# Kernel tuning notes

Hardware: AMD Instinct MI355X
Metric: run time of the kernel (lower is better)

The kernel has to match this reference:

```python
import jax, jax.numpy as jnp
import numpy as np

N_NODES = 100_000
N_EDGES = 1_200_000
IN_C, HID_C, OUT_C, K = 64, 64, 32, 3


def setup_inputs() -> dict:
    key = jax.random.key(0)
    ks = jax.random.split(key, 8)
    x = jax.random.normal(ks[0], (N_NODES, IN_C), dtype=jnp.float32)
    edge_index = jax.random.randint(ks[1], (2, N_EDGES), 0, N_NODES, dtype=jnp.int64)
    # ChebConv parameters: weight [K, in, out], bias [out] (Glorot-ish scale)
    W1 = jax.random.normal(ks[2], (K, IN_C, HID_C), dtype=jnp.float32) / np.sqrt(IN_C)
    b1 = jnp.zeros((HID_C,), dtype=jnp.float32)
    W2 = jax.random.normal(ks[3], (K, HID_C, OUT_C), dtype=jnp.float32) / np.sqrt(HID_C)
    b2 = jnp.zeros((OUT_C,), dtype=jnp.float32)
    return {"x": x, "edge_index": edge_index, "W1": W1, "b1": b1, "W2": W2, "b2": b2}


def _cheb_conv(x, row, col, norm_w, W, b):
    # Scaled Laplacian with lambda_max=2 (PyG default): L_hat = -D^{-1/2} A D^{-1/2}
    def prop(t):  # L_hat @ t, via edge gather + segment-sum scatter
        msg = norm_w[:, None] * t[col]            # [E, C]
        return -jax.ops.segment_sum(msg, row, num_segments=N_NODES)

    Tx0 = x
    out = Tx0 @ W[0]
    Tx1 = prop(x)
    out = out + Tx1 @ W[1]
    for k in range(2, W.shape[0]):
        Tx2 = 2.0 * prop(Tx1) - Tx0          # Chebyshev recurrence
        out = out + Tx2 @ W[k]
        Tx0, Tx1 = Tx1, Tx2
    return out + b


def reference(x, edge_index, W1, b1, W2, b2):
    row, col = edge_index[0], edge_index[1]
    deg = jax.ops.segment_sum(jnp.ones((row.shape[0],), x.dtype), row,
                              num_segments=N_NODES)
    deg_inv_sqrt = jnp.where(deg > 0, jax.lax.rsqrt(jnp.maximum(deg, 1.0)), 0.0)
    norm_w = deg_inv_sqrt[row] * deg_inv_sqrt[col]   # symmetric normalization

    h = jax.nn.relu(_cheb_conv(x, row, col, norm_w, W1, b1))
    # dropout omitted (eval mode / training=False)
    return _cheb_conv(h, row, col, norm_w, W2, b2)
```

## Files before the change

kernel.cpp:

```cpp
#include <hip/hip_runtime.h>
#include <hip/hip_fp16.h>

#define N_NODES_C 100000
#define N_EDGES_C 1200000
#define NBUK ((N_NODES_C + 255) >> 8)
#define CHUNK 4096

typedef _Float16 f16x8 __attribute__((ext_vector_type(8)));
typedef float f32x4 __attribute__((ext_vector_type(4)));

#define PACK(r8, c) ((c) | ((r8) << 17))
#define UNPACK_C(v) ((v) & 0x1FFFF)
#define UNPACK_R(v) ((v) >> 17)

__global__ __launch_bounds__(256) void hist_f2h(const int* __restrict__ ei,
                                                int* __restrict__ bucket_cnt,
                                                const float* __restrict__ x,
                                                __half* __restrict__ xh,
                                                int nedges, int n4, int histB) {
    __shared__ int cnt[NBUK];
    const int tid = threadIdx.x;
    if (blockIdx.x < histB) {
        const int base = blockIdx.x * CHUNK;
        const int nloc = min(CHUNK, nedges - base);
        for (int i = tid; i < NBUK; i += 256) cnt[i] = 0;
        __syncthreads();
        for (int i = tid; i < nloc; i += 256) atomicAdd(&cnt[ei[base + i] >> 8], 1);
        __syncthreads();
        for (int b = tid; b < NBUK; b += 256) {
            int n = cnt[b];
            if (n) atomicAdd(&bucket_cnt[b], n);
        }
    } else {
        int i = (blockIdx.x - histB) * 256 + tid;
        if (i < n4) {
            float4 v = ((const float4*)x)[i];
            __half2 tmp[2];
            tmp[0] = __floats2half2_rn(v.x, v.y);
            tmp[1] = __floats2half2_rn(v.z, v.w);
            ((float2*)xh)[i] = *(float2*)tmp;
        }
    }
}

__global__ __launch_bounds__(256) void scan_fold(const int* __restrict__ bucket_cnt,
                                                 int* __restrict__ bucket_base,
                                                 int* __restrict__ bucket_next, int nb,
                                                 const float* __restrict__ W1,
                                                 const float* __restrict__ W2,
                                                 __half* __restrict__ W1f,
                                                 __half* __restrict__ W2f) {
    const int tid = threadIdx.x;
    if (blockIdx.x == 0) {
        __shared__ int s[256];
        int a0 = (2 * tid < nb) ? bucket_cnt[2 * tid] : 0;
        int a1 = (2 * tid + 1 < nb) ? bucket_cnt[2 * tid + 1] : 0;
        s[tid] = a0 + a1;
        __syncthreads();
        for (int off = 1; off < 256; off <<= 1) {
            int v = s[tid];
            int add = (tid >= off) ? s[tid - off] : 0;
            __syncthreads();
            s[tid] = v + add;
            __syncthreads();
        }
        int excl = (tid > 0) ? s[tid - 1] : 0;
        if (2 * tid < nb) { bucket_base[2 * tid] = excl; bucket_next[2 * tid] = excl; }
        if (2 * tid + 1 < nb) { bucket_base[2 * tid + 1] = excl + a0; bucket_next[2 * tid + 1] = excl + a0; }
        if (tid == 255) bucket_base[nb] = s[255];
        return;
    }
    int i = (blockIdx.x - 1) * 256 + tid;
    if (i < 12288) {
        int j = i & 7;
        int lane = (i >> 3) & 63;
        int rest = i >> 9;
        int kh = rest % 6;
        int ct = rest / 6;
        int term = kh >> 1;
        int k = ((kh & 1) << 5) | ((lane >> 4) << 3) | j;
        int c = (ct << 4) | (lane & 15);
        float w0 = W1[k * 64 + c];
        float w1 = W1[4096 + k * 64 + c];
        float w2 = W1[2 * 4096 + k * 64 + c];
        float v = (term == 0) ? (w0 - w2) : ((term == 1) ? w1 : 2.0f * w2);
        W1f[i] = __float2half(v);
    } else if (i < 12288 + 6144) {
        int ii = i - 12288;
        int j = ii & 7;
        int lane = (ii >> 3) & 63;
        int rest = ii >> 9;
        int kh = rest & 1;
        int ct = rest >> 1;
        int k = (kh << 5) | ((lane >> 4) << 3) | j;
        int cg = ct * 16 + (lane & 15);
        int seg = cg >> 5;
        int c = cg & 31;
        float w0 = W2[k * 32 + c];
        float w1 = W2[2048 + k * 32 + c];
        float w2 = W2[2 * 2048 + k * 32 + c];
        float v = (seg == 0) ? (w0 - w2) : ((seg == 1) ? w1 : 2.0f * w2);
        W2f[ii] = __float2half(v);
    }
}

__global__ __launch_bounds__(256) void bin_stage(const int* __restrict__ ei,
                                                 int* __restrict__ bucket_next,
                                                 int* __restrict__ staged, int nedges) {
    __shared__ int cnt[NBUK];
    __shared__ int ofs[NBUK];
    __shared__ int run[NBUK];
    __shared__ int gbase[NBUK];
    __shared__ int ssum[256];
    __shared__ int2 sedge[CHUNK];
    const int tid = threadIdx.x;
    const int base = blockIdx.x * CHUNK;
    const int nloc = min(CHUNK, nedges - base);

    for (int i = tid; i < NBUK; i += 256) { cnt[i] = 0; run[i] = 0; }
    __syncthreads();

    int r[16], c[16];
#pragma unroll
    for (int k = 0; k < 16; ++k) {
        int loc = tid + k * 256;
        bool ok = loc < nloc;
        int idx = base + loc;
        r[k] = ok ? ei[idx] : -1;
        c[k] = ok ? ei[nedges + idx] : 0;
        if (ok) atomicAdd(&cnt[r[k] >> 8], 1);
    }
    __syncthreads();

    int a0 = (2 * tid < NBUK) ? cnt[2 * tid] : 0;
    int a1 = (2 * tid + 1 < NBUK) ? cnt[2 * tid + 1] : 0;
    ssum[tid] = a0 + a1;
    __syncthreads();
    for (int off = 1; off < 256; off <<= 1) {
        int v = ssum[tid];
        int add = (tid >= off) ? ssum[tid - off] : 0;
        __syncthreads();
        ssum[tid] = v + add;
        __syncthreads();
    }
    int excl = (tid > 0) ? ssum[tid - 1] : 0;
    if (2 * tid < NBUK) ofs[2 * tid] = excl;
    if (2 * tid + 1 < NBUK) ofs[2 * tid + 1] = excl + a0;
    __syncthreads();

#pragma unroll
    for (int k = 0; k < 16; ++k) {
        if (r[k] >= 0) {
            int b = r[k] >> 8;
            int p = atomicAdd(&run[b], 1);
            sedge[ofs[b] + p] = make_int2(r[k], c[k]);
        }
    }
    __syncthreads();

    for (int b = tid; b < NBUK; b += 256) {
        int n = cnt[b];
        gbase[b] = n ? atomicAdd(&bucket_next[b], n) : 0;
    }
    __syncthreads();

    for (int i = tid; i < nloc; i += 256) {
        int2 e = sedge[i];
        int b = e.x >> 8;
        staged[gbase[b] + (i - ofs[b])] = PACK(e.x & 255, e.y);
    }
}

__global__ __launch_bounds__(256) void bin_count(const int* __restrict__ staged,
                                                 const int* __restrict__ bucket_base,
                                                 int* __restrict__ rowptr, float* __restrict__ dis,
                                                 int nnodes, int nedges) {
    __shared__ int deg[256];
    __shared__ int ssum[256];
    const int b = blockIdx.x;
    const int n0 = b << 8;
    const int nend = min(n0 + 256, nnodes);
    const int nloc = nend - n0;
    const int tid = threadIdx.x;
    deg[tid] = 0;
    __syncthreads();
    const int ebase = bucket_base[b];
    const int ecount = bucket_base[b + 1] - ebase;
    for (int i = tid; i < ecount; i += 256) {
        atomicAdd(&deg[UNPACK_R(staged[ebase + i])], 1);
    }
    __syncthreads();
    int d = deg[tid];
    if (tid < nloc) {
        float df = (float)d;
        dis[n0 + tid] = (d > 0) ? (1.0f / sqrtf(fmaxf(df, 1.f))) : 0.f;
    }
    ssum[tid] = d;
    __syncthreads();
    for (int off = 1; off < 256; off <<= 1) {
        int v = ssum[tid];
        int add = (tid >= off) ? ssum[tid - off] : 0;
        __syncthreads();
        ssum[tid] = v + add;
        __syncthreads();
    }
    int excl = (tid > 0) ? ssum[tid - 1] : 0;
    if (tid < nloc) rowptr[n0 + tid] = ebase + excl;
    if (b == NBUK - 1 && tid == 0) rowptr[nnodes] = nedges;
}

__global__ __launch_bounds__(256) void bin_place(const int* __restrict__ staged,
                                                 const int* __restrict__ rowptr,
                                                 const float* __restrict__ dis,
                                                 int2* __restrict__ colw, int nnodes) {
    __shared__ int rp[256];
    __shared__ int nx[256];
    __shared__ float dl[256];
    const int b = blockIdx.x;
    const int n0 = b << 8;
    const int nend = min(n0 + 256, nnodes);
    const int nloc = nend - n0;
    const int tid = threadIdx.x;
    if (tid < nloc) {
        rp[tid] = rowptr[n0 + tid];
        dl[tid] = dis[n0 + tid];
    }
    nx[tid] = 0;
    __syncthreads();
    const int ebase = rowptr[n0];
    const int ecount = rowptr[nend] - ebase;
    for (int i = tid; i < ecount; i += 256) {
        int v = staged[ebase + i];
        int col = UNPACK_C(v);
        int rrel = UNPACK_R(v);
        int p = atomicAdd(&nx[rrel], 1);
        float w = -dl[rrel] * dis[col];
        colw[rp[rrel] + p] = make_int2(col, __float_as_int(w));
    }
}

__global__ __launch_bounds__(256) void prop_gather_h(const __half* __restrict__ t,
                                                     const int* __restrict__ rowptr,
                                                     const int2* __restrict__ colw,
                                                     __half* __restrict__ out, int nnodes) {
    int grp = threadIdx.x >> 3;
    int ln = threadIdx.x & 7;
    int node = blockIdx.x * 32 + grp;
    if (node >= nnodes) return;
    int s = rowptr[node];
    int e = rowptr[node + 1];
    float acc[8] = {0.f, 0.f, 0.f, 0.f, 0.f, 0.f, 0.f, 0.f};
    int i = s;
    for (; i + 3 < e; i += 4) {
        int2 cw0 = colw[i];
        int2 cw1 = colw[i + 1];
        int2 cw2 = colw[i + 2];
        int2 cw3 = colw[i + 3];
        float4 r0 = ((const float4*)(t + (size_t)cw0.x * 64))[ln];
        float4 r1 = ((const float4*)(t + (size_t)cw1.x * 64))[ln];
        float4 r2 = ((const float4*)(t + (size_t)cw2.x * 64))[ln];
        float4 r3 = ((const float4*)(t + (size_t)cw3.x * 64))[ln];
        float w0 = __int_as_float(cw0.y);
        float w1 = __int_as_float(cw1.y);
        float w2 = __int_as_float(cw2.y);
        float w3 = __int_as_float(cw3.y);
        const __half2* h0 = (const __half2*)&r0;
        const __half2* h1 = (const __half2*)&r1;
        const __half2* h2 = (const __half2*)&r2;
        const __half2* h3 = (const __half2*)&r3;
#pragma unroll
        for (int q = 0; q < 4; ++q) {
            float2 f0 = __half22float2(h0[q]);
            float2 f1 = __half22float2(h1[q]);
            float2 f2 = __half22float2(h2[q]);
            float2 f3 = __half22float2(h3[q]);
            acc[2 * q + 0] += w0 * f0.x + w1 * f1.x + w2 * f2.x + w3 * f3.x;
            acc[2 * q + 1] += w0 * f0.y + w1 * f1.y + w2 * f2.y + w3 * f3.y;
        }
    }
    for (; i < e; ++i) {
        int2 cw0 = colw[i];
        float w0 = __int_as_float(cw0.y);
        float4 r0 = ((const float4*)(t + (size_t)cw0.x * 64))[ln];
        const __half2* h0 = (const __half2*)&r0;
#pragma unroll
        for (int q = 0; q < 4; ++q) {
            float2 f0 = __half22float2(h0[q]);
            acc[2 * q + 0] += w0 * f0.x;
            acc[2 * q + 1] += w0 * f0.y;
        }
    }
    __half2 tmp[4];
    tmp[0] = __floats2half2_rn(acc[0], acc[1]);
    tmp[1] = __floats2half2_rn(acc[2], acc[3]);
    tmp[2] = __floats2half2_rn(acc[4], acc[5]);
    tmp[3] = __floats2half2_rn(acc[6], acc[7]);
    ((float4*)(out + (size_t)node * 64))[ln] = *(float4*)tmp;
}

template <bool F32OUT>
__global__ __launch_bounds__(256) void prop_gather32(const __half* __restrict__ t,
                                                     const int* __restrict__ rowptr,
                                                     const int2* __restrict__ colw,
                                                     const void* __restrict__ addin,
                                                     void* __restrict__ outv, int nnodes) {
    int grp = threadIdx.x >> 2;
    int ln = threadIdx.x & 3;
    int node = blockIdx.x * 64 + grp;
    if (node >= nnodes) return;
    int s = rowptr[node];
    int e = rowptr[node + 1];
    float acc[8] = {0.f, 0.f, 0.f, 0.f, 0.f, 0.f, 0.f, 0.f};
    int i = s;
    for (; i + 3 < e; i += 4) {
        int2 cw0 = colw[i];
        int2 cw1 = colw[i + 1];
        int2 cw2 = colw[i + 2];
        int2 cw3 = colw[i + 3];
        float4 r0 = ((const float4*)(t + (size_t)cw0.x * 32))[ln];
        float4 r1 = ((const float4*)(t + (size_t)cw1.x * 32))[ln];
        float4 r2 = ((const float4*)(t + (size_t)cw2.x * 32))[ln];
        float4 r3 = ((const float4*)(t + (size_t)cw3.x * 32))[ln];
        float w0 = __int_as_float(cw0.y);
        float w1 = __int_as_float(cw1.y);
        float w2 = __int_as_float(cw2.y);
        float w3 = __int_as_float(cw3.y);
        const __half2* h0 = (const __half2*)&r0;
        const __half2* h1 = (const __half2*)&r1;
        const __half2* h2 = (const __half2*)&r2;
        const __half2* h3 = (const __half2*)&r3;
#pragma unroll
        for (int q = 0; q < 4; ++q) {
            float2 f0 = __half22float2(h0[q]);
            float2 f1 = __half22float2(h1[q]);
            float2 f2 = __half22float2(h2[q]);
            float2 f3 = __half22float2(h3[q]);
            acc[2 * q + 0] += w0 * f0.x + w1 * f1.x + w2 * f2.x + w3 * f3.x;
            acc[2 * q + 1] += w0 * f0.y + w1 * f1.y + w2 * f2.y + w3 * f3.y;
        }
    }
    for (; i < e; ++i) {
        int2 cw0 = colw[i];
        float w0 = __int_as_float(cw0.y);
        float4 r0 = ((const float4*)(t + (size_t)cw0.x * 32))[ln];
        const __half2* h0 = (const __half2*)&r0;
#pragma unroll
        for (int q = 0; q < 4; ++q) {
            float2 f0 = __half22float2(h0[q]);
            acc[2 * q + 0] += w0 * f0.x;
            acc[2 * q + 1] += w0 * f0.y;
        }
    }
    if (F32OUT) {
        const float* add = (const float*)addin;
        float* out = (float*)outv;
        float4 a0 = ((const float4*)(add + (size_t)node * 32))[ln * 2 + 0];
        float4 a1 = ((const float4*)(add + (size_t)node * 32))[ln * 2 + 1];
        a0.x += acc[0]; a0.y += acc[1]; a0.z += acc[2]; a0.w += acc[3];
        a1.x += acc[4]; a1.y += acc[5]; a1.z += acc[6]; a1.w += acc[7];
        ((float4*)(out + (size_t)node * 32))[ln * 2 + 0] = a0;
        ((float4*)(out + (size_t)node * 32))[ln * 2 + 1] = a1;
    } else {
        const __half* add = (const __half*)addin;
        __half* out = (__half*)outv;
        float4 raw = ((const float4*)(add + (size_t)node * 32))[ln];
        const __half2* hp = (const __half2*)&raw;
        float2 a0 = __half22float2(hp[0]);
        float2 a1 = __half22float2(hp[1]);
        float2 a2 = __half22float2(hp[2]);
        float2 a3 = __half22float2(hp[3]);
        __half2 tmp[4];
        tmp[0] = __floats2half2_rn(acc[0] + a0.x, acc[1] + a0.y);
        tmp[1] = __floats2half2_rn(acc[2] + a1.x, acc[3] + a1.y);
        tmp[2] = __floats2half2_rn(acc[4] + a2.x, acc[5] + a2.y);
        tmp[3] = __floats2half2_rn(acc[6] + a3.x, acc[7] + a3.y);
        ((float4*)(out + (size_t)node * 32))[ln] = *(float4*)tmp;
    }
}

__global__ __launch_bounds__(256) void gemm_fused(const __half* __restrict__ A0,
                                                  const __half* __restrict__ A1,
                                                  const __half* __restrict__ A2,
                                                  const __half* __restrict__ W1f,
                                                  const float* __restrict__ b1,
                                                  const __half* __restrict__ W2f,
                                                  const float* __restrict__ b2,
                                                  float* __restrict__ P0,
                                                  __half* __restrict__ G1,
                                                  __half* __restrict__ G2, int nnodes) {
    __shared__ __align__(16) __half htile[4][16 * 72];
    const int wave = threadIdx.x >> 6;
    const int lane = threadIdx.x & 63;
    const int node0 = blockIdx.x * 64 + wave * 16;
    const int m = lane & 15;
    const int quad = lane >> 4;
    int arow = node0 + m;
    if (arow >= nnodes) arow = nnodes - 1;

    const __half* Ap[3] = {A0, A1, A2};
    f16x8 a[6];
#pragma unroll
    for (int kh = 0; kh < 6; ++kh) {
        const __half* A = Ap[kh >> 1];
        a[kh] = *(const f16x8*)(A + (size_t)arow * 64 + ((kh & 1) << 5) + (quad << 3));
    }
    __half* ht = htile[wave];
#pragma unroll
    for (int ct = 0; ct < 4; ++ct) {
        f32x4 acc = {0.f, 0.f, 0.f, 0.f};
#pragma unroll
        for (int kh = 0; kh < 6; ++kh) {
            f16x8 b = *(const f16x8*)(W1f + ((size_t)(ct * 6 + kh) * 64 + lane) * 8);
            acc = __builtin_amdgcn_mfma_f32_16x16x32_f16(a[kh], b, acc, 0, 0, 0);
        }
        int col = (ct << 4) | m;
        float bias = b1[col];
#pragma unroll
        for (int r = 0; r < 4; ++r) {
            ht[(quad * 4 + r) * 72 + col] = __float2half(fmaxf(acc[r] + bias, 0.f));
        }
    }
    __syncthreads();

    f16x8 h0 = *(const f16x8*)(ht + m * 72 + (quad << 3));
    f16x8 h1 = *(const f16x8*)(ht + m * 72 + 32 + (quad << 3));
#pragma unroll
    for (int ct = 0; ct < 6; ++ct) {
        f32x4 acc = {0.f, 0.f, 0.f, 0.f};
        f16x8 b0 = *(const f16x8*)(W2f + ((size_t)(ct * 2 + 0) * 64 + lane) * 8);
        f16x8 b1v = *(const f16x8*)(W2f + ((size_t)(ct * 2 + 1) * 64 + lane) * 8);
        acc = __builtin_amdgcn_mfma_f32_16x16x32_f16(h0, b0, acc, 0, 0, 0);
        acc = __builtin_amdgcn_mfma_f32_16x16x32_f16(h1, b1v, acc, 0, 0, 0);
        int seg = ct >> 1;
        int c = ((ct & 1) << 4) | m;
#pragma unroll
        for (int r = 0; r < 4; ++r) {
            int n = node0 + (quad << 2) + r;
            if (n >= nnodes) continue;
            float v = acc[r];
            if (seg == 0)      P0[(size_t)n * 32 + c] = v + b2[c];
            else if (seg == 1) G1[(size_t)n * 32 + c] = __float2half(v);
            else               G2[(size_t)n * 32 + c] = __float2half(v);
        }
    }
}

extern "C" void kernel_launch(void* const* d_in, const int* in_sizes, int n_in,
                              void* d_out, int out_size, void* d_ws, size_t ws_size,
                              hipStream_t stream) {
    const float* x  = (const float*)d_in[0];
    const int*   ei = (const int*)d_in[1];
    const float* W1 = (const float*)d_in[2];
    const float* b1 = (const float*)d_in[3];
    const float* W2 = (const float*)d_in[4];
    const float* b2 = (const float*)d_in[5];
    float* out = (float*)d_out;

    const int NN = N_NODES_C;
    const int NE = N_EDGES_C;
    const size_t HFEAT_BYTES = (size_t)NN * 64 * sizeof(__half);
    const size_t H32_BYTES = (size_t)NN * 32 * sizeof(__half);

    char* ws = (char*)d_ws;
    size_t off = 0;
    auto alloc = [&](size_t bytes) -> void* {
        void* p = ws + off;
        off += (bytes + 255) & ~(size_t)255;
        return p;
    };
    int*    bucket_cnt  = (int*)alloc((size_t)NBUK * 4);
    int*    bucket_base = (int*)alloc((size_t)(NBUK + 1) * 4);
    int*    bucket_next = (int*)alloc((size_t)NBUK * 4);
    int*    rowptr      = (int*)alloc((size_t)(NN + 1) * 4);
    float*  dis         = (float*)alloc((size_t)NN * 4);
    int*    staged      = (int*)alloc((size_t)NE * 4);
    int2*   colw        = (int2*)alloc((size_t)NE * 8);
    __half* xh          = (__half*)alloc(HFEAT_BYTES);
    __half* T1h         = (__half*)alloc(HFEAT_BYTES);
    __half* T2h         = (__half*)alloc(HFEAT_BYTES);
    __half* Qh          = (__half*)alloc(H32_BYTES);
    float*  P0          = (float*)alloc((size_t)NN * 32 * 4);
    __half* W1f         = (__half*)alloc((size_t)4 * 6 * 64 * 8 * 2);
    __half* W2f         = (__half*)alloc((size_t)6 * 2 * 64 * 8 * 2);

    const int PROPB = (NN + 31) / 32;
    const int PROP32B = (NN + 63) / 64;
    const int CONV4 = NN * 64 / 4;
    const int CONVB = (CONV4 + 255) / 256;
    const int BINB = (NE + CHUNK - 1) / CHUNK;
    const int GEMMB = (NN + 63) / 64;
    const int FOLDB = 1 + (18432 + 255) / 256;

    hipMemsetAsync(bucket_cnt, 0, (size_t)NBUK * 4, stream);
    hist_f2h<<<BINB + CONVB, 256, 0, stream>>>(ei, bucket_cnt, x, xh, NE, CONV4, BINB);
    scan_fold<<<FOLDB, 256, 0, stream>>>(bucket_cnt, bucket_base, bucket_next, NBUK,
                                         W1, W2, W1f, W2f);
    bin_stage<<<BINB, 256, 0, stream>>>(ei, bucket_next, staged, NE);
    bin_count<<<NBUK, 256, 0, stream>>>(staged, bucket_base, rowptr, dis, NN, NE);
    bin_place<<<NBUK, 256, 0, stream>>>(staged, rowptr, dis, colw, NN);

    prop_gather_h<<<PROPB, 256, 0, stream>>>(xh, rowptr, colw, T1h, NN);
    prop_gather_h<<<PROPB, 256, 0, stream>>>(T1h, rowptr, colw, T2h, NN);
    gemm_fused<<<GEMMB, 256, 0, stream>>>(xh, T1h, T2h, W1f, b1, W2f, b2, P0, T1h, T2h, NN);

    prop_gather32<false><<<PROP32B, 256, 0, stream>>>(T2h, rowptr, colw, T1h, Qh, NN);
    prop_gather32<true><<<PROP32B, 256, 0, stream>>>(Qh, rowptr, colw, P0, out, NN);
}
```

Before: 244.8 us.

## Compute node degrees with global atomics in histogram pass, merge count and place kernels

Node degrees are now accumulated with global atomics during the first histogram pass over edges, and the inverse square root of degree is computed in the scan/fold kernel. This removes the separate bin_count kernel, which re-read the staged edges, and folds the per-bucket rowptr scan into the placement kernel. The aim is to drop one launch and one full pass over the staged array. The cost is 1.2M scattered global atomics on a 100K-entry array plus a larger memset.

Result: slower. 277.0 us (+13.2%).

```diff
diff --git a/kernel.cpp b/kernel.cpp
--- a/kernel.cpp
+++ b/kernel.cpp
@@ -13,11 +13,12 @@
 #define UNPACK_C(v) ((v) & 0x1FFFF)
 #define UNPACK_R(v) ((v) >> 17)
 
-__global__ __launch_bounds__(256) void hist_f2h(const int* __restrict__ ei,
-                                                int* __restrict__ bucket_cnt,
-                                                const float* __restrict__ x,
-                                                __half* __restrict__ xh,
-                                                int nedges, int n4, int histB) {
+__global__ __launch_bounds__(256) void hist_deg_f2h(const int* __restrict__ ei,
+                                                    int* __restrict__ bucket_cnt,
+                                                    int* __restrict__ deg,
+                                                    const float* __restrict__ x,
+                                                    __half* __restrict__ xh,
+                                                    int nedges, int n4, int histB) {
     __shared__ int cnt[NBUK];
     const int tid = threadIdx.x;
     if (blockIdx.x < histB) {
@@ -25,7 +26,11 @@
         const int nloc = min(CHUNK, nedges - base);
         for (int i = tid; i < NBUK; i += 256) cnt[i] = 0;
         __syncthreads();
-        for (int i = tid; i < nloc; i += 256) atomicAdd(&cnt[ei[base + i] >> 8], 1);
+        for (int i = tid; i < nloc; i += 256) {
+            int r = ei[base + i];
+            atomicAdd(&cnt[r >> 8], 1);
+            atomicAdd(&deg[r], 1);
+        }
         __syncthreads();
         for (int b = tid; b < NBUK; b += 256) {
             int n = cnt[b];
@@ -43,13 +48,15 @@
     }
 }
 
-__global__ __launch_bounds__(256) void scan_fold(const int* __restrict__ bucket_cnt,
-                                                 int* __restrict__ bucket_base,
-                                                 int* __restrict__ bucket_next, int nb,
-                                                 const float* __restrict__ W1,
-                                                 const float* __restrict__ W2,
-                                                 __half* __restrict__ W1f,
-                                                 __half* __restrict__ W2f) {
+__global__ __launch_bounds__(256) void scan_fold_dis(const int* __restrict__ bucket_cnt,
+                                                     int* __restrict__ bucket_base,
+                                                     int* __restrict__ bucket_next, int nb,
+                                                     const float* __restrict__ W1,
+                                                     const float* __restrict__ W2,
+                                                     __half* __restrict__ W1f,
+                                                     __half* __restrict__ W2f,
+                                                     const int* __restrict__ deg,
+                                                     float* __restrict__ dis, int nnodes) {
     const int tid = threadIdx.x;
     if (blockIdx.x == 0) {
         __shared__ int s[256];
@@ -101,6 +108,13 @@
         float w2 = W2[2 * 2048 + k * 32 + c];
         float v = (seg == 0) ? (w0 - w2) : ((seg == 1) ? w1 : 2.0f * w2);
         W2f[ii] = __float2half(v);
+    } else {
+        int n = i - 18432;
+        if (n < nnodes) {
+            int d = deg[n];
+            float df = (float)d;
+            dis[n] = (d > 0) ? (1.0f / sqrtf(fmaxf(df, 1.f))) : 0.f;
+        }
     }
 }
 
@@ -171,48 +185,14 @@
     }
 }
 
-__global__ __launch_bounds__(256) void bin_count(const int* __restrict__ staged,
-                                                 const int* __restrict__ bucket_base,
-                                                 int* __restrict__ rowptr, float* __restrict__ dis,
-                                                 int nnodes, int nedges) {
-    __shared__ int deg[256];
+__global__ __launch_bounds__(256) void rowptr_place(const int* __restrict__ staged,
+                                                    const int* __restrict__ bucket_base,
+                                                    const int* __restrict__ deg,
+                                                    const float* __restrict__ dis,
+                                                    int* __restrict__ rowptr,
+                                                    int2* __restrict__ colw,
+                                                    int nnodes, int nedges) {
     __shared__ int ssum[256];
-    const int b = blockIdx.x;
-    const int n0 = b << 8;
-    const int nend = min(n0 + 256, nnodes);
-    const int nloc = nend - n0;
-    const int tid = threadIdx.x;
-    deg[tid] = 0;
-    __syncthreads();
-    const int ebase = bucket_base[b];
-    const int ecount = bucket_base[b + 1] - ebase;
-    for (int i = tid; i < ecount; i += 256) {
-        atomicAdd(&deg[UNPACK_R(staged[ebase + i])], 1);
-    }
-    __syncthreads();
-    int d = deg[tid];
-    if (tid < nloc) {
-        float df = (float)d;
-        dis[n0 + tid] = (d > 0) ? (1.0f / sqrtf(fmaxf(df, 1.f))) : 0.f;
-    }
-    ssum[tid] = d;
-    __syncthreads();
-    for (int off = 1; off < 256; off <<= 1) {
-        int v = ssum[tid];
-        int add = (tid >= off) ? ssum[tid - off] : 0;
-        __syncthreads();
-        ssum[tid] = v + add;
-        __syncthreads();
-    }
-    int excl = (tid > 0) ? ssum[tid - 1] : 0;
-    if (tid < nloc) rowptr[n0 + tid] = ebase + excl;
-    if (b == NBUK - 1 && tid == 0) rowptr[nnodes] = nedges;
-}
-
-__global__ __launch_bounds__(256) void bin_place(const int* __restrict__ staged,
-                                                 const int* __restrict__ rowptr,
-                                                 const float* __restrict__ dis,
-                                                 int2* __restrict__ colw, int nnodes) {
     __shared__ int rp[256];
     __shared__ int nx[256];
     __shared__ float dl[256];
@@ -221,14 +201,25 @@
     const int nend = min(n0 + 256, nnodes);
     const int nloc = nend - n0;
     const int tid = threadIdx.x;
-    if (tid < nloc) {
-        rp[tid] = rowptr[n0 + tid];
-        dl[tid] = dis[n0 + tid];
-    }
+    int d = (tid < nloc) ? deg[n0 + tid] : 0;
+    if (tid < nloc) dl[tid] = dis[n0 + tid];
     nx[tid] = 0;
-    __syncthreads();
-    const int ebase = rowptr[n0];
-    const int ecount = rowptr[nend] - ebase;
+    ssum[tid] = d;
+    __syncthreads();
+    for (int off = 1; off < 256; off <<= 1) {
+        int v = ssum[tid];
+        int add = (tid >= off) ? ssum[tid - off] : 0;
+        __syncthreads();
+        ssum[tid] = v + add;
+        __syncthreads();
+    }
+    int excl = (tid > 0) ? ssum[tid - 1] : 0;
+    const int ebase = bucket_base[b];
+    rp[tid] = ebase + excl;
+    if (tid < nloc) rowptr[n0 + tid] = ebase + excl;
+    if (b == NBUK - 1 && tid == 0) rowptr[nnodes] = nedges;
+    __syncthreads();
+    const int ecount = bucket_base[b + 1] - ebase;
     for (int i = tid; i < ecount; i += 256) {
         int v = staged[ebase + i];
         int col = UNPACK_C(v);
@@ -469,6 +460,7 @@
         return p;
     };
     int*    bucket_cnt  = (int*)alloc((size_t)NBUK * 4);
+    int*    deg         = (int*)alloc((size_t)NN * 4);
     int*    bucket_base = (int*)alloc((size_t)(NBUK + 1) * 4);
     int*    bucket_next = (int*)alloc((size_t)NBUK * 4);
     int*    rowptr      = (int*)alloc((size_t)(NN + 1) * 4);
@@ -489,15 +481,17 @@
     const int CONVB = (CONV4 + 255) / 256;
     const int BINB = (NE + CHUNK - 1) / CHUNK;
     const int GEMMB = (NN + 63) / 64;
-    const int FOLDB = 1 + (18432 + 255) / 256;
-
-    hipMemsetAsync(bucket_cnt, 0, (size_t)NBUK * 4, stream);
-    hist_f2h<<<BINB + CONVB, 256, 0, stream>>>(ei, bucket_cnt, x, xh, NE, CONV4, BINB);
-    scan_fold<<<FOLDB, 256, 0, stream>>>(bucket_cnt, bucket_base, bucket_next, NBUK,
-                                         W1, W2, W1f, W2f);
+    const int FOLDB = 1 + (18432 + N_NODES_C + 255) / 256;
+
+    size_t zbytes = (size_t)((char*)bucket_base - (char*)bucket_cnt);
+    hipMemsetAsync(bucket_cnt, 0, zbytes, stream);
+    hist_deg_f2h<<<BINB + CONVB, 256, 0, stream>>>(ei, bucket_cnt, deg, x, xh,
+                                                   NE, CONV4, BINB);
+    scan_fold_dis<<<FOLDB, 256, 0, stream>>>(bucket_cnt, bucket_base, bucket_next, NBUK,
+                                             W1, W2, W1f, W2f, deg, dis, NN);
     bin_stage<<<BINB, 256, 0, stream>>>(ei, bucket_next, staged, NE);
-    bin_count<<<NBUK, 256, 0, stream>>>(staged, bucket_base, rowptr, dis, NN, NE);
-    bin_place<<<NBUK, 256, 0, stream>>>(staged, rowptr, dis, colw, NN);
+    rowptr_place<<<NBUK, 256, 0, stream>>>(staged, bucket_base, deg, dis,
+                                           rowptr, colw, NN, NE);
 
     prop_gather_h<<<PROPB, 256, 0, stream>>>(xh, rowptr, colw, T1h, NN);
     prop_gather_h<<<PROPB, 256, 0, stream>>>(T1h, rowptr, colw, T2h, NN);
```
